# Kernel tuning notes

Hardware: AMD Instinct MI355X
Metric: run time of the kernel (lower is better)

The kernel has to match this reference:

```python
import jax, jax.numpy as jnp
import numpy as np

INPUT_CLIP_RATIO = 1.0  # init kwarg
QMIN, QMAX = -8, 7      # signed int4 range


def setup_inputs() -> dict:
    key = jax.random.key(0)
    x = jax.random.normal(key, (8192, 4096), dtype=jnp.float32)
    return {"x": x}


def reference(x):
    # flatten leading dims: [num_tokens, hidden]
    x2 = x.reshape(-1, x.shape[-1]).astype(jnp.float32)
    # per-token max-abs scale: max|x| / 7 * clip_ratio
    scales = jnp.max(jnp.abs(x2), axis=-1) / 7.0 * INPUT_CLIP_RATIO  # [N]
    # quantize to signed int4
    q = jnp.clip(jnp.round(x2 / scales[:, None]), QMIN, QMAX).astype(jnp.int32)
    # pack two int4 values per int8 byte: even index -> low nibble, odd -> high nibble
    low = q[:, 0::2] & 0xF
    high = q[:, 1::2] & 0xF
    packed = ((high << 4) | low).astype(jnp.int8)  # [N, hidden//2]
    return packed, scales
```

## Files before the change

### kernel.cpp

```cpp
#include <hip/hip_runtime.h>


constexpr int TOKENS  = 8192;
constexpr int HIDDEN  = 4096;
constexpr int THREADS = 256;
constexpr int F4_THR  = HIDDEN / 4 / THREADS;
constexpr int PACKED_ROW = HIDDEN / 2;
constexpr long long PACKED_TOTAL = (long long)TOKENS * PACKED_ROW;

__global__ __launch_bounds__(THREADS) void quant_i4_kernel(
    const float* __restrict__ x, float* __restrict__ out) {
  const int row = blockIdx.x;
  const int t   = threadIdx.x;
  const float* __restrict__ xrow = x + (size_t)row * HIDDEN;

  float4 v[F4_THR];
  float m = 0.0f;
#pragma unroll
  for (int k = 0; k < F4_THR; ++k) {
    v[k] = reinterpret_cast<const float4*>(xrow)[t + k * THREADS];
    m = fmaxf(m, fmaxf(fmaxf(fabsf(v[k].x), fabsf(v[k].y)),
                       fmaxf(fabsf(v[k].z), fabsf(v[k].w))));
  }

#pragma unroll
  for (int off = 32; off >= 1; off >>= 1)
    m = fmaxf(m, __shfl_xor(m, off));

  __shared__ float smax[THREADS / 64];
  if ((t & 63) == 0) smax[t >> 6] = m;
  __syncthreads();
  const float M = fmaxf(fmaxf(smax[0], smax[1]), fmaxf(smax[2], smax[3]));

  const float rcp7  = (float)(1.0 / 7.0);
  const float scale = M * rcp7;
  const double sD   = (double)scale;
  const float  rcp  = (float)(1.0 / sD);

  float* __restrict__ orow = out + (size_t)row * PACKED_ROW;
#pragma unroll
  for (int k = 0; k < F4_THR; ++k) {
    float xs[4] = {v[k].x, v[k].y, v[k].z, v[k].w};
    int qi[4];
#pragma unroll
    for (int j = 0; j < 4; ++j) {
      float a = xs[j] * rcp;
      float r = rintf(a);
      if (0.5f - fabsf(a - r) < 1e-5f) {
        r = rintf((float)((double)xs[j] / sD));
      }
      r = fminf(fmaxf(r, -8.0f), 7.0f);
      qi[j] = (int)r;
    }
    float2 w;
    w.x = (float)(signed char)(((qi[1] & 0xF) << 4) | (qi[0] & 0xF));
    w.y = (float)(signed char)(((qi[3] & 0xF) << 4) | (qi[2] & 0xF));
    reinterpret_cast<float2*>(orow)[k * THREADS + t] = w;
  }

  if (t == 0) out[PACKED_TOTAL + row] = scale;
}

extern "C" void kernel_launch(void* const* d_in, const int* in_sizes, int n_in,
                              void* d_out, int out_size, void* d_ws, size_t ws_size,
                              hipStream_t stream) {
  const float* x = (const float*)d_in[0];
  float* out = (float*)d_out;
  quant_i4_kernel<<<TOKENS, THREADS, 0, stream>>>(x, out);
}
```

Measured before the change: 205.9 us.

## Map one wavefront per row and store packed output as float4

Each 64-lane wavefront now owns a full row, so each block handles four rows. This drops the shared-memory reduction and __syncthreads in favor of a wave-only shuffle reduction. Each lane loads two adjacent float4s per step, letting it emit four packed outputs with a single 16-byte store instead of 8-byte stores. Register use rises to 16 float4s per thread, which may lower occupancy, and each lane's load pattern becomes strided by two float4s.

```diff
diff --git a/kernel.cpp b/kernel.cpp
--- a/kernel.cpp
+++ b/kernel.cpp
@@ -4,46 +4,47 @@
 constexpr int TOKENS  = 8192;
 constexpr int HIDDEN  = 4096;
 constexpr int THREADS = 256;
-constexpr int F4_THR  = HIDDEN / 4 / THREADS;
+constexpr int ROWS_PER_BLOCK = THREADS / 64;
+constexpr int BLOCKS  = TOKENS / ROWS_PER_BLOCK;
 constexpr int PACKED_ROW = HIDDEN / 2;
 constexpr long long PACKED_TOTAL = (long long)TOKENS * PACKED_ROW;
 
 __global__ __launch_bounds__(THREADS) void quant_i4_kernel(
     const float* __restrict__ x, float* __restrict__ out) {
-  const int row = blockIdx.x;
-  const int t   = threadIdx.x;
+  const int wave = threadIdx.x >> 6;
+  const int lane = threadIdx.x & 63;
+  const int row  = blockIdx.x * ROWS_PER_BLOCK + wave;
   const float* __restrict__ xrow = x + (size_t)row * HIDDEN;
 
-  float4 v[F4_THR];
+  float4 v[16];
   float m = 0.0f;
 #pragma unroll
-  for (int k = 0; k < F4_THR; ++k) {
-    v[k] = reinterpret_cast<const float4*>(xrow)[t + k * THREADS];
-    m = fmaxf(m, fmaxf(fmaxf(fabsf(v[k].x), fabsf(v[k].y)),
-                       fmaxf(fabsf(v[k].z), fabsf(v[k].w))));
+  for (int p = 0; p < 8; ++p) {
+    v[2 * p]     = reinterpret_cast<const float4*>(xrow)[2 * lane + 128 * p];
+    v[2 * p + 1] = reinterpret_cast<const float4*>(xrow)[2 * lane + 1 + 128 * p];
+    m = fmaxf(m, fmaxf(fmaxf(fabsf(v[2 * p].x), fabsf(v[2 * p].y)),
+                       fmaxf(fabsf(v[2 * p].z), fabsf(v[2 * p].w))));
+    m = fmaxf(m, fmaxf(fmaxf(fabsf(v[2 * p + 1].x), fabsf(v[2 * p + 1].y)),
+                       fmaxf(fabsf(v[2 * p + 1].z), fabsf(v[2 * p + 1].w))));
   }
 
 #pragma unroll
   for (int off = 32; off >= 1; off >>= 1)
     m = fmaxf(m, __shfl_xor(m, off));
 
-  __shared__ float smax[THREADS / 64];
-  if ((t & 63) == 0) smax[t >> 6] = m;
-  __syncthreads();
-  const float M = fmaxf(fmaxf(smax[0], smax[1]), fmaxf(smax[2], smax[3]));
-
-  const float rcp7  = (float)(1.0 / 7.0);
-  const float scale = M * rcp7;
-  const double sD   = (double)scale;
-  const float  rcp  = (float)(1.0 / sD);
+  const float  rcp7  = (float)(1.0 / 7.0);
+  const float  scale = m * rcp7;
+  const double sD    = (double)scale;
+  const float  rcp   = (float)(1.0 / sD);
 
   float* __restrict__ orow = out + (size_t)row * PACKED_ROW;
 #pragma unroll
-  for (int k = 0; k < F4_THR; ++k) {
-    float xs[4] = {v[k].x, v[k].y, v[k].z, v[k].w};
-    int qi[4];
+  for (int p = 0; p < 8; ++p) {
+    float xs[8] = {v[2 * p].x,     v[2 * p].y,     v[2 * p].z,     v[2 * p].w,
+                   v[2 * p + 1].x, v[2 * p + 1].y, v[2 * p + 1].z, v[2 * p + 1].w};
+    int qi[8];
 #pragma unroll
-    for (int j = 0; j < 4; ++j) {
+    for (int j = 0; j < 8; ++j) {
       float a = xs[j] * rcp;
       float r = rintf(a);
       if (0.5f - fabsf(a - r) < 1e-5f) {
@@ -52,13 +53,15 @@
       r = fminf(fmaxf(r, -8.0f), 7.0f);
       qi[j] = (int)r;
     }
-    float2 w;
+    float4 w;
     w.x = (float)(signed char)(((qi[1] & 0xF) << 4) | (qi[0] & 0xF));
     w.y = (float)(signed char)(((qi[3] & 0xF) << 4) | (qi[2] & 0xF));
-    reinterpret_cast<float2*>(orow)[k * THREADS + t] = w;
+    w.z = (float)(signed char)(((qi[5] & 0xF) << 4) | (qi[4] & 0xF));
+    w.w = (float)(signed char)(((qi[7] & 0xF) << 4) | (qi[6] & 0xF));
+    reinterpret_cast<float4*>(orow)[lane + 64 * p] = w;
   }
 
-  if (t == 0) out[PACKED_TOTAL + row] = scale;
+  if (lane == 0) out[PACKED_TOTAL + row] = scale;
 }
 
 extern "C" void kernel_launch(void* const* d_in, const int* in_sizes, int n_in,
@@ -66,5 +69,5 @@
                               hipStream_t stream) {
   const float* x = (const float*)d_in[0];
   float* out = (float*)d_out;
-  quant_i4_kernel<<<TOKENS, THREADS, 0, stream>>>(x, out);
+  quant_i4_kernel<<<BLOCKS, THREADS, 0, stream>>>(x, out);
 }
```

Result: slower. 211.4 us (+2.7%).
